# Kernel optimization log

Measured on AMD Instinct MI355X. Metric: run time of the kernel, lower is better.

The kernel has to match this reference:

```python
import jax, jax.numpy as jnp
import numpy as np

N = 2048        # tokens (batch*seq)
H = 4096        # hidden_size (LLaMA-7B)
I = 11008       # intermediate_size (LLaMA-7B)
QMAX = 127.0    # int8 symmetric quant range


def setup_inputs() -> dict:
    key = jax.random.key(0)
    ks = jax.random.split(key, 6)
    # pre-quantized int8 activations (stored as int32) + per-token dynamic scales
    x_q = jax.random.randint(ks[0], (N, H), -127, 128, dtype=jnp.int32)
    x_scale = jax.random.uniform(ks[1], (N,), dtype=jnp.float32) * 0.01 + 1e-4
    # fused [gate; up] int8 weight [2I, H] with per-output-channel scales
    w_gateup = jax.random.randint(ks[2], (2 * I, H), -127, 128, dtype=jnp.int32)
    w_gateup_scale = jax.random.uniform(ks[3], (2 * I,), dtype=jnp.float32) * 0.005 + 1e-4
    # down_proj int8 weight [H, I] with per-output-channel scales
    w_down = jax.random.randint(ks[4], (H, I), -127, 128, dtype=jnp.int32)
    w_down_scale = jax.random.uniform(ks[5], (H,), dtype=jnp.float32) * 0.005 + 1e-4
    return {"x_q": x_q, "x_scale": x_scale, "w_gateup": w_gateup,
            "w_gateup_scale": w_gateup_scale, "w_down": w_down,
            "w_down_scale": w_down_scale}


def reference(x_q, x_scale, w_gateup, w_gateup_scale, w_down, w_down_scale):
    acc = jnp.matmul(x_q, w_gateup.T)                      # [N, 2I] int32
    gateup = acc.astype(jnp.float32) * x_scale[:, None] * w_gateup_scale[None, :]
    # --- fused silu_and_mul + dynamic per-token requantization ---
    gate, up = jnp.split(gateup, 2, axis=-1)               # each [N, I]
    act = jax.nn.silu(gate) * up                           # [N, I]
    s2 = jnp.max(jnp.abs(act), axis=-1) / QMAX             # [N] dynamic scale
    q2 = jnp.clip(jnp.round(act / s2[:, None]), -QMAX, QMAX)  # requantized int8 (as f32)
    out = jnp.matmul(q2, w_down.T.astype(jnp.float32)) * s2[:, None] * w_down_scale[None, :]
    return out                                             # [N, H]
```

## Files before the change

### kernel.cpp

```cpp
#include <hip/hip_runtime.h>
#include <stdint.h>

typedef int i32x4 __attribute__((ext_vector_type(4)));
typedef unsigned short u16x8 __attribute__((ext_vector_type(8)));

#define N_TOK 2048
#define HID   4096
#define INTER 11008
#define TWOI  22016
#define KT1   64
#define KT2   172

#define GLD16(gp, lp) __builtin_amdgcn_global_load_lds( \
    (const __attribute__((address_space(1))) void*)(gp), \
    (__attribute__((address_space(3))) void*)(lp), 16, 0, 0)
#define BAR() __builtin_amdgcn_s_barrier()
#define WVM(n) asm volatile("s_waitcnt vmcnt(" #n ")" ::: "memory")
#define LGKM0() do { asm volatile("s_waitcnt lgkmcnt(0)" ::: "memory"); \
                     __builtin_amdgcn_sched_barrier(0); } while (0)

__device__ __forceinline__ unsigned short f2bf(float f) {
  uint32_t u = __float_as_uint(f);
  uint32_t r = (u + 0x7fffu + ((u >> 16) & 1u)) >> 16;
  return (unsigned short)r;
}

__device__ __forceinline__ float bf2f(unsigned short b) {
  return __uint_as_float(((uint32_t)b) << 16);
}

__global__ __launch_bounds__(256) void pack_panel3(
    const int* __restrict__ src, uint8_t* __restrict__ dst,
    int lgPR, int KT, int K)
{
  const int u = blockIdx.x * 256 + threadIdx.x;
  const int q = u & 3;
  const int r2 = u >> 2;
  const int rl = r2 & ((1 << lgPR) - 1);
  const int s = r2 >> lgPR;
  const int p = s / KT;
  const int t = s - p * KT;
  const int row = (p << lgPR) + rl;
  const int col = t * 64 + ((q ^ (rl & 3)) << 4);
  const int* sp = src + (size_t)row * K + col;
  i32x4 o;
#pragma unroll
  for (int qq = 0; qq < 4; ++qq) {
    i32x4 w = *reinterpret_cast<const i32x4*>(sp + qq * 4);
    o[qq] = (w[0] & 255) | ((w[1] & 255) << 8) | ((w[2] & 255) << 16)
          | ((w[3] & 255) << 24);
  }
  *reinterpret_cast<i32x4*>(dst + (size_t)u * 16) = o;
}

__global__ __launch_bounds__(512, 2) void gemm1_k(
    const uint8_t* __restrict__ x8p, const uint8_t* __restrict__ wgp,
    const float* __restrict__ xs, const float* __restrict__ wgs,
    unsigned short* __restrict__ gu)
{
  __shared__ uint8_t sm[98304];
  const int tid = threadIdx.x;
  const int lane = tid & 63, wid = tid >> 6;
  const int wgm = wid >> 2, wgn = wid & 3;
  const int r15 = lane & 15;
  const int slotC = (((lane >> 4) ^ (r15 & 3)) << 4);

  const int bid = blockIdx.x;
  const int v = (bid & 7) * 172 + (bid >> 3);
  const int mt = v & 15;
  const int ntB = v >> 4;

  const uint8_t* pA = x8p + (size_t)mt  * (KT1 * 8192)  + tid * 16;
  const uint8_t* pB = wgp + (size_t)ntB * (KT1 * 16384) + tid * 16;

  const int arow = (wgm << 6) + r15;
  const int brow = (wgn << 6) + r15;
  i32x4 acc[4][4] = {};

#define STG1(t, s) do {                                        \
    uint8_t* l = sm + (s) * 24576 + tid * 16;                  \
    GLD16(pA + (size_t)(t) * 8192, l);                         \
    const uint8_t* bb = pB + (size_t)(t) * 16384;              \
    GLD16(bb, l + 8192);                                       \
    GLD16(bb + 8192, l + 16384);                               \
  } while (0)

  STG1(0, 0); STG1(1, 1); STG1(2, 2);
  WVM(6); BAR();

  for (int t = 0; t < KT1; ++t) {
    const int rem = KT1 - 1 - t;
    const uint8_t* b = sm + (t & 3) * 24576;
    uint8_t* lnx = sm + ((t + 3) & 3) * 24576 + tid * 16;
    i32x4 bv[4], av[2];
#pragma unroll
    for (int n = 0; n < 4; ++n)
      bv[n] = *reinterpret_cast<const i32x4*>(
          b + 8192 + (brow + n * 16) * 64 + slotC);
#pragma unroll
    for (int m = 0; m < 2; ++m)
      av[m] = *reinterpret_cast<const i32x4*>(b + (arow + m * 16) * 64 + slotC);
    if (rem >= 3) {
      const uint8_t* bb = pB + (size_t)(t + 3) * 16384;
      GLD16(bb, lnx + 8192);
      GLD16(bb + 8192, lnx + 16384);
    }
    BAR();
    LGKM0();
    __builtin_amdgcn_s_setprio(1);
#pragma unroll
    for (int m = 0; m < 2; ++m)
#pragma unroll
      for (int n = 0; n < 4; ++n)
        acc[m][n] = __builtin_amdgcn_mfma_i32_16x16x64_i8(
            av[m], bv[n], acc[m][n], 0, 0, 0);
    __builtin_amdgcn_s_setprio(0);
#pragma unroll
    for (int m = 0; m < 2; ++m)
      av[m] = *reinterpret_cast<const i32x4*>(
          b + (arow + (m + 2) * 16) * 64 + slotC);
    if (rem >= 3) {
      GLD16(pA + (size_t)(t + 3) * 8192, lnx);
      WVM(6);
    } else if (rem == 2) { WVM(3); }
    else if (rem == 1)   { WVM(0); }
    BAR();
    LGKM0();
    __builtin_amdgcn_s_setprio(1);
#pragma unroll
    for (int m = 0; m < 2; ++m)
#pragma unroll
      for (int n = 0; n < 4; ++n)
        acc[m + 2][n] = __builtin_amdgcn_mfma_i32_16x16x64_i8(
            av[m], bv[n], acc[m + 2][n], 0, 0, 0);
    __builtin_amdgcn_s_setprio(0);
  }
#undef STG1

  const int rq = (lane >> 4) << 2;
#pragma unroll
  for (int m = 0; m < 4; ++m) {
#pragma unroll
    for (int r = 0; r < 4; ++r) {
      const int rowl = (wgm << 6) + m * 16 + rq + r;
      const int grow = mt * 128 + rowl;
      const float xr = xs[grow];
      const int colb = ntB * 256 + (wgn << 6) + r15;
      unsigned short* op = gu + (size_t)grow * TWOI + colb;
      const float* wp = wgs + colb;
#pragma unroll
      for (int n = 0; n < 4; ++n)
        op[n * 16] = f2bf((float)acc[m][n][r] * xr * wp[n * 16]);
    }
  }
}

__global__ __launch_bounds__(256) void rowmax_k(
    const unsigned short* __restrict__ gu, float* __restrict__ mx)
{
  const int row = blockIdx.x;
  const unsigned short* gp = gu + (size_t)row * TWOI;
  float m = 0.f;
  for (int i = threadIdx.x; i < INTER / 8; i += 256) {
    u16x8 gv = *reinterpret_cast<const u16x8*>(gp + i * 8);
    u16x8 uv = *reinterpret_cast<const u16x8*>(gp + INTER + i * 8);
#pragma unroll
    for (int j = 0; j < 8; ++j) {
      float gf = bf2f(gv[j]);
      float uf = bf2f(uv[j]);
      float a = (gf / (1.f + __expf(-gf))) * uf;
      m = fmaxf(m, __builtin_fabsf(a));
    }
  }
#pragma unroll
  for (int o = 32; o; o >>= 1) m = fmaxf(m, __shfl_xor(m, o, 64));
  __shared__ float red[4];
  const int lane = threadIdx.x & 63, wid = threadIdx.x >> 6;
  if (lane == 0) red[wid] = m;
  __syncthreads();
  if (threadIdx.x == 0)
    mx[row] = fmaxf(fmaxf(red[0], red[1]), fmaxf(red[2], red[3]));
}

__global__ __launch_bounds__(256) void quant_k(
    const unsigned short* __restrict__ gu, const float* __restrict__ mx,
    uint8_t* __restrict__ q2p)
{
  const int u = blockIdx.x * 256 + threadIdx.x;
  const int q = u & 3;
  const int rl = (u >> 2) & 127;
  const int s = u >> 9;
  const int mt = s / KT2;
  const int t = s - mt * KT2;
  const int row = mt * 128 + rl;
  const int col = t * 64 + ((q ^ (rl & 3)) << 4);
  const unsigned short* gp = gu + (size_t)row * TWOI + col;
  const float inv = 127.0f / fmaxf(mx[row], 1e-30f);
  u16x8 g0 = *reinterpret_cast<const u16x8*>(gp);
  u16x8 g1 = *reinterpret_cast<const u16x8*>(gp + 8);
  u16x8 u0 = *reinterpret_cast<const u16x8*>(gp + INTER);
  u16x8 u1 = *reinterpret_cast<const u16x8*>(gp + INTER + 8);
  i32x4 o;
#pragma unroll
  for (int qq = 0; qq < 4; ++qq) {
    uint32_t d = 0;
#pragma unroll
    for (int b = 0; b < 4; ++b) {
      const int j = qq * 4 + b;
      float gf = bf2f((j < 8) ? g0[j] : g1[j - 8]);
      float uf = bf2f((j < 8) ? u0[j] : u1[j - 8]);
      float a = (gf / (1.f + __expf(-gf))) * uf;
      float rr = rintf(a * inv);
      rr = fminf(fmaxf(rr, -127.f), 127.f);
      d |= ((uint32_t)((int)rr & 255)) << (8 * b);
    }
    o[qq] = (int)d;
  }
  *reinterpret_cast<i32x4*>(q2p + (size_t)u * 16) = o;
}

__global__ __launch_bounds__(512, 2) void gemm2_k(
    const uint8_t* __restrict__ q2p, const uint8_t* __restrict__ wdp,
    const float* __restrict__ mx, const float* __restrict__ wds,
    float* __restrict__ out)
{
  __shared__ uint8_t sm[98304];
  const int tid = threadIdx.x;
  const int lane = tid & 63, wid = tid >> 6;
  const int wgm = wid >> 2, wgn = wid & 3;
  const int r15 = lane & 15;
  const int slotC = (((lane >> 4) ^ (r15 & 3)) << 4);

  const int bid = blockIdx.x;
  const int v = (bid & 7) * 32 + (bid >> 3);
  const int nt = v >> 4, mt = v & 15;

  const uint8_t* pA = q2p + (size_t)mt * (KT2 * 8192)  + tid * 16;
  const uint8_t* pB = wdp + (size_t)nt * (KT2 * 16384) + tid * 16;

  const int arow = (wgm << 6) + r15;
  const int brow = (wgn << 6) + r15;
  i32x4 acc[4][4] = {};

#define STG2(t, s) do {                                        \
    uint8_t* l = sm + (s) * 24576 + tid * 16;                  \
    GLD16(pA + (size_t)(t) * 8192, l);                         \
    const uint8_t* bb = pB + (size_t)(t) * 16384;              \
    GLD16(bb, l + 8192);                                       \
    GLD16(bb + 8192, l + 16384);                               \
  } while (0)

  STG2(0, 0); STG2(1, 1); STG2(2, 2);
  WVM(6); BAR();

  for (int t = 0; t < KT2; ++t) {
    const int rem = KT2 - 1 - t;
    const uint8_t* b = sm + (t & 3) * 24576;
    uint8_t* lnx = sm + ((t + 3) & 3) * 24576 + tid * 16;
    i32x4 bv[4], av[2];
#pragma unroll
    for (int n = 0; n < 4; ++n)
      bv[n] = *reinterpret_cast<const i32x4*>(
          b + 8192 + (brow + n * 16) * 64 + slotC);
#pragma unroll
    for (int m = 0; m < 2; ++m)
      av[m] = *reinterpret_cast<const i32x4*>(b + (arow + m * 16) * 64 + slotC);
    if (rem >= 3) {
      const uint8_t* bb = pB + (size_t)(t + 3) * 16384;
      GLD16(bb, lnx + 8192);
      GLD16(bb + 8192, lnx + 16384);
    }
    BAR();
    LGKM0();
    __builtin_amdgcn_s_setprio(1);
#pragma unroll
    for (int m = 0; m < 2; ++m)
#pragma unroll
      for (int n = 0; n < 4; ++n)
        acc[m][n] = __builtin_amdgcn_mfma_i32_16x16x64_i8(
            av[m], bv[n], acc[m][n], 0, 0, 0);
    __builtin_amdgcn_s_setprio(0);
#pragma unroll
    for (int m = 0; m < 2; ++m)
      av[m] = *reinterpret_cast<const i32x4*>(
          b + (arow + (m + 2) * 16) * 64 + slotC);
    if (rem >= 3) {
      GLD16(pA + (size_t)(t + 3) * 8192, lnx);
      WVM(6);
    } else if (rem == 2) { WVM(3); }
    else if (rem == 1)   { WVM(0); }
    BAR();
    LGKM0();
    __builtin_amdgcn_s_setprio(1);
#pragma unroll
    for (int m = 0; m < 2; ++m)
#pragma unroll
      for (int n = 0; n < 4; ++n)
        acc[m + 2][n] = __builtin_amdgcn_mfma_i32_16x16x64_i8(
            av[m], bv[n], acc[m + 2][n], 0, 0, 0);
    __builtin_amdgcn_s_setprio(0);
  }
#undef STG2

  const int rq = (lane >> 4) << 2;
#pragma unroll
  for (int m = 0; m < 4; ++m) {
#pragma unroll
    for (int r = 0; r < 4; ++r) {
      const int rowl = (wgm << 6) + m * 16 + rq + r;
      const int grow = mt * 128 + rowl;
      const float s2 = mx[grow] * (1.0f / 127.0f);
      float* op = out + (size_t)grow * HID + nt * 256 + (wgn << 6) + r15;
      const float* wp = wds + nt * 256 + (wgn << 6) + r15;
#pragma unroll
      for (int n = 0; n < 4; ++n)
        op[n * 16] = (float)acc[m][n][r] * s2 * wp[n * 16];
    }
  }
}

extern "C" void kernel_launch(void* const* d_in, const int* in_sizes, int n_in,
                              void* d_out, int out_size, void* d_ws, size_t ws_size,
                              hipStream_t stream)
{
  const int*   x_q = (const int*)d_in[0];
  const float* xs  = (const float*)d_in[1];
  const int*   wg  = (const int*)d_in[2];
  const float* wgs = (const float*)d_in[3];
  const int*   wd  = (const int*)d_in[4];
  const float* wds = (const float*)d_in[5];
  float* out = (float*)d_out;

  uint8_t* ws = (uint8_t*)d_ws;
  uint8_t* x8p = ws;
  uint8_t* wgp = x8p + 8388608;
  uint8_t* wdp = wgp + 90177536;
  unsigned short* gu = (unsigned short*)(wdp + 45088768);
  float* mx = (float*)((uint8_t*)gu + 90177536);
  uint8_t* q2p = (uint8_t*)mx + 8192;

  pack_panel3<<<2048, 256, 0, stream>>>(x_q, x8p, 7, KT1, HID);
  pack_panel3<<<22016, 256, 0, stream>>>(wg, wgp, 8, KT1, HID);
  pack_panel3<<<11008, 256, 0, stream>>>(wd, wdp, 8, KT2, INTER);

  gemm1_k<<<1376, 512, 0, stream>>>(x8p, wgp, xs, wgs, gu);
  rowmax_k<<<N_TOK, 256, 0, stream>>>(gu, mx);
  quant_k<<<5504, 256, 0, stream>>>(gu, mx, q2p);
  gemm2_k<<<256, 512, 0, stream>>>(q2p, wdp, mx, wds, out);
}
```

Measured before the change: 473.2 us.

## Double-buffer LDS fragments in registers and use one barrier per k-step

Both int8 GEMM main loops are restructured into a ping-pong register pipeline. The A/B fragments for tile t+1 are read from LDS while the MFMAs for tile t run on the other register set, and each k-step issues all 16 MFMAs back to back. The two barriers and explicit lgkmcnt waits per step become a single barrier, with a coarser vmcnt wait on the global-to-LDS staging. This is meant to hide LDS read latency and cut synchronisation overhead, at the cost of extra VGPRs for the second fragment set and a loop that relies on an even K-tile count.

```diff
diff --git a/kernel.cpp b/kernel.cpp
--- a/kernel.cpp
+++ b/kernel.cpp
@@ -16,8 +16,6 @@
     (__attribute__((address_space(3))) void*)(lp), 16, 0, 0)
 #define BAR() __builtin_amdgcn_s_barrier()
 #define WVM(n) asm volatile("s_waitcnt vmcnt(" #n ")" ::: "memory")
-#define LGKM0() do { asm volatile("s_waitcnt lgkmcnt(0)" ::: "memory"); \
-                     __builtin_amdgcn_sched_barrier(0); } while (0)
 
 __device__ __forceinline__ unsigned short f2bf(float f) {
   uint32_t u = __float_as_uint(f);
@@ -53,6 +51,40 @@
   *reinterpret_cast<i32x4*>(dst + (size_t)u * 16) = o;
 }
 
+#define RDQ(SET, tt) do {                                            \
+    const uint8_t* bn = sm + ((tt) & 3) * 24576;                     \
+    _Pragma("unroll")                                                \
+    for (int n = 0; n < 4; ++n)                                      \
+      bv##SET[n] = *reinterpret_cast<const i32x4*>(                  \
+          bn + 8192 + (brow + n * 16) * 64 + slotC);                 \
+    _Pragma("unroll")                                                \
+    for (int m = 0; m < 4; ++m)                                      \
+      av##SET[m] = *reinterpret_cast<const i32x4*>(                  \
+          bn + (arow + m * 16) * 64 + slotC);                        \
+  } while (0)
+
+#define MMQ(SET) do {                                                \
+    __builtin_amdgcn_s_setprio(1);                                   \
+    _Pragma("unroll")                                                \
+    for (int m = 0; m < 4; ++m)                                      \
+      _Pragma("unroll")                                              \
+      for (int n = 0; n < 4; ++n)                                    \
+        acc[m][n] = __builtin_amdgcn_mfma_i32_16x16x64_i8(           \
+            av##SET[m], bv##SET[n], acc[m][n], 0, 0, 0);             \
+    __builtin_amdgcn_s_setprio(0);                                   \
+  } while (0)
+
+#define STEPQ(KT, t, CUR, NXT) do {                                  \
+    const int rem = (KT) - 1 - (t);                                  \
+    if ((t) + 1 < (KT)) RDQ(NXT, (t) + 1);                           \
+    if (rem >= 3) STG((t) + 3, ((t) + 3) & 3);                       \
+    __builtin_amdgcn_sched_barrier(0);                               \
+    MMQ(CUR);                                                        \
+    if (rem >= 3)      { WVM(3); }                                   \
+    else if (rem == 2) { WVM(0); }                                   \
+    BAR();                                                           \
+  } while (0)
+
 __global__ __launch_bounds__(512, 2) void gemm1_k(
     const uint8_t* __restrict__ x8p, const uint8_t* __restrict__ wgp,
     const float* __restrict__ xs, const float* __restrict__ wgs,
@@ -76,8 +108,9 @@
   const int arow = (wgm << 6) + r15;
   const int brow = (wgn << 6) + r15;
   i32x4 acc[4][4] = {};
-
-#define STG1(t, s) do {                                        \
+  i32x4 av0[4], bv0[4], av1[4], bv1[4];
+
+#define STG(t, s) do {                                         \
     uint8_t* l = sm + (s) * 24576 + tid * 16;                  \
     GLD16(pA + (size_t)(t) * 8192, l);                         \
     const uint8_t* bb = pB + (size_t)(t) * 16384;              \
@@ -85,57 +118,15 @@
     GLD16(bb + 8192, l + 16384);                               \
   } while (0)
 
-  STG1(0, 0); STG1(1, 1); STG1(2, 2);
-  WVM(6); BAR();
-
-  for (int t = 0; t < KT1; ++t) {
-    const int rem = KT1 - 1 - t;
-    const uint8_t* b = sm + (t & 3) * 24576;
-    uint8_t* lnx = sm + ((t + 3) & 3) * 24576 + tid * 16;
-    i32x4 bv[4], av[2];
-#pragma unroll
-    for (int n = 0; n < 4; ++n)
-      bv[n] = *reinterpret_cast<const i32x4*>(
-          b + 8192 + (brow + n * 16) * 64 + slotC);
-#pragma unroll
-    for (int m = 0; m < 2; ++m)
-      av[m] = *reinterpret_cast<const i32x4*>(b + (arow + m * 16) * 64 + slotC);
-    if (rem >= 3) {
-      const uint8_t* bb = pB + (size_t)(t + 3) * 16384;
-      GLD16(bb, lnx + 8192);
-      GLD16(bb + 8192, lnx + 16384);
-    }
-    BAR();
-    LGKM0();
-    __builtin_amdgcn_s_setprio(1);
-#pragma unroll
-    for (int m = 0; m < 2; ++m)
-#pragma unroll
-      for (int n = 0; n < 4; ++n)
-        acc[m][n] = __builtin_amdgcn_mfma_i32_16x16x64_i8(
-            av[m], bv[n], acc[m][n], 0, 0, 0);
-    __builtin_amdgcn_s_setprio(0);
-#pragma unroll
-    for (int m = 0; m < 2; ++m)
-      av[m] = *reinterpret_cast<const i32x4*>(
-          b + (arow + (m + 2) * 16) * 64 + slotC);
-    if (rem >= 3) {
-      GLD16(pA + (size_t)(t + 3) * 8192, lnx);
-      WVM(6);
-    } else if (rem == 2) { WVM(3); }
-    else if (rem == 1)   { WVM(0); }
-    BAR();
-    LGKM0();
-    __builtin_amdgcn_s_setprio(1);
-#pragma unroll
-    for (int m = 0; m < 2; ++m)
-#pragma unroll
-      for (int n = 0; n < 4; ++n)
-        acc[m + 2][n] = __builtin_amdgcn_mfma_i32_16x16x64_i8(
-            av[m], bv[n], acc[m + 2][n], 0, 0, 0);
-    __builtin_amdgcn_s_setprio(0);
-  }
-#undef STG1
+  STG(0, 0); STG(1, 1); STG(2, 2);
+  WVM(3); BAR();
+  RDQ(0, 0);
+
+  for (int t = 0; t < KT1; t += 2) {
+    STEPQ(KT1, t, 0, 1);
+    STEPQ(KT1, t + 1, 1, 0);
+  }
+#undef STG
 
   const int rq = (lane >> 4) << 2;
 #pragma unroll
@@ -241,8 +232,9 @@
   const int arow = (wgm << 6) + r15;
   const int brow = (wgn << 6) + r15;
   i32x4 acc[4][4] = {};
-
-#define STG2(t, s) do {                                        \
+  i32x4 av0[4], bv0[4], av1[4], bv1[4];
+
+#define STG(t, s) do {                                         \
     uint8_t* l = sm + (s) * 24576 + tid * 16;                  \
     GLD16(pA + (size_t)(t) * 8192, l);                         \
     const uint8_t* bb = pB + (size_t)(t) * 16384;              \
@@ -250,57 +242,15 @@
     GLD16(bb + 8192, l + 16384);                               \
   } while (0)
 
-  STG2(0, 0); STG2(1, 1); STG2(2, 2);
-  WVM(6); BAR();
-
-  for (int t = 0; t < KT2; ++t) {
-    const int rem = KT2 - 1 - t;
-    const uint8_t* b = sm + (t & 3) * 24576;
-    uint8_t* lnx = sm + ((t + 3) & 3) * 24576 + tid * 16;
-    i32x4 bv[4], av[2];
-#pragma unroll
-    for (int n = 0; n < 4; ++n)
-      bv[n] = *reinterpret_cast<const i32x4*>(
-          b + 8192 + (brow + n * 16) * 64 + slotC);
-#pragma unroll
-    for (int m = 0; m < 2; ++m)
-      av[m] = *reinterpret_cast<const i32x4*>(b + (arow + m * 16) * 64 + slotC);
-    if (rem >= 3) {
-      const uint8_t* bb = pB + (size_t)(t + 3) * 16384;
-      GLD16(bb, lnx + 8192);
-      GLD16(bb + 8192, lnx + 16384);
-    }
-    BAR();
-    LGKM0();
-    __builtin_amdgcn_s_setprio(1);
-#pragma unroll
-    for (int m = 0; m < 2; ++m)
-#pragma unroll
-      for (int n = 0; n < 4; ++n)
-        acc[m][n] = __builtin_amdgcn_mfma_i32_16x16x64_i8(
-            av[m], bv[n], acc[m][n], 0, 0, 0);
-    __builtin_amdgcn_s_setprio(0);
-#pragma unroll
-    for (int m = 0; m < 2; ++m)
-      av[m] = *reinterpret_cast<const i32x4*>(
-          b + (arow + (m + 2) * 16) * 64 + slotC);
-    if (rem >= 3) {
-      GLD16(pA + (size_t)(t + 3) * 8192, lnx);
-      WVM(6);
-    } else if (rem == 2) { WVM(3); }
-    else if (rem == 1)   { WVM(0); }
-    BAR();
-    LGKM0();
-    __builtin_amdgcn_s_setprio(1);
-#pragma unroll
-    for (int m = 0; m < 2; ++m)
-#pragma unroll
-      for (int n = 0; n < 4; ++n)
-        acc[m + 2][n] = __builtin_amdgcn_mfma_i32_16x16x64_i8(
-            av[m], bv[n], acc[m + 2][n], 0, 0, 0);
-    __builtin_amdgcn_s_setprio(0);
-  }
-#undef STG2
+  STG(0, 0); STG(1, 1); STG(2, 2);
+  WVM(3); BAR();
+  RDQ(0, 0);
+
+  for (int t = 0; t < KT2; t += 2) {
+    STEPQ(KT2, t, 0, 1);
+    STEPQ(KT2, t + 1, 1, 0);
+  }
+#undef STG
 
   const int rq = (lane >> 4) << 2;
 #pragma unroll
```

Result: no change. 481.3 us (+1.7%).
